# Performance work log

Hardware: AMD Instinct MI355X
Metric: run time of the kernel (lower is better)

The kernel has to match this reference:

```python
import jax, jax.numpy as jnp
import numpy as np

C_CT, C_MRI, C_OUT = 64, 64, 64
B, D, H, W = 1, 8, 32, 32


def setup_inputs() -> dict:
    key = jax.random.key(0)
    ks = jax.random.split(key, 18)
    s = 0.05
    inp = {
        "ct_features": jax.random.normal(ks[0], (B, C_CT, D, H, W), jnp.float32),
        "mri_features": jax.random.normal(ks[1], (B, C_MRI, D, H, W), jnp.float32),
        # 1x1x1 Conv3d == per-voxel linear: weight (out, in), bias (out,)
        "wq_ct": jax.random.normal(ks[2], (C_OUT, C_CT), jnp.float32) * s,
        "bq_ct": jax.random.normal(ks[3], (C_OUT,), jnp.float32) * s,
        "wk_mri": jax.random.normal(ks[4], (C_OUT, C_MRI), jnp.float32) * s,
        "bk_mri": jax.random.normal(ks[5], (C_OUT,), jnp.float32) * s,
        "wv_mri": jax.random.normal(ks[6], (C_OUT, C_MRI), jnp.float32) * s,
        "bv_mri": jax.random.normal(ks[7], (C_OUT,), jnp.float32) * s,
        "wq_mri": jax.random.normal(ks[8], (C_OUT, C_MRI), jnp.float32) * s,
        "bq_mri": jax.random.normal(ks[9], (C_OUT,), jnp.float32) * s,
        "wk_ct": jax.random.normal(ks[10], (C_OUT, C_CT), jnp.float32) * s,
        "bk_ct": jax.random.normal(ks[11], (C_OUT,), jnp.float32) * s,
        "wv_ct": jax.random.normal(ks[12], (C_OUT, C_CT), jnp.float32) * s,
        "bv_ct": jax.random.normal(ks[13], (C_OUT,), jnp.float32) * s,
        "wo": jax.random.normal(ks[14], (C_OUT, 2 * C_OUT), jnp.float32) * s,
        "bo": jax.random.normal(ks[15], (C_OUT,), jnp.float32) * s,
    }
    return inp


def _proj(x_flat, w, b):
    # x_flat: (B, Cin, N); 1x1x1 conv -> (B, Cout, N)
    return jnp.einsum("oc,bcn->bon", w, x_flat) + b[None, :, None]


def _forward(ct, mri, wq_ct, bq_ct, wk_mri, bk_mri, wv_mri, bv_mri,
             wq_mri, bq_mri, wk_ct, bk_ct, wv_ct, bv_ct, wo, bo):
    b, _, d, h, w = ct.shape
    n = d * h * w
    ct_f = ct.reshape(b, ct.shape[1], n)
    mri_f = mri.reshape(b, mri.shape[1], n)
    scale = 1.0 / np.sqrt(C_OUT).astype(np.float32)

    # CT queries attend over MRI keys/values
    ct_q = _proj(ct_f, wq_ct, bq_ct)      # (B, C, N)
    mri_k = _proj(mri_f, wk_mri, bk_mri)  # (B, C, N)
    mri_v = _proj(mri_f, wv_mri, bv_mri)  # (B, C, N)
    attn_ct = jax.nn.softmax(jnp.einsum("bci,bcj->bij", ct_q, mri_k) * scale, axis=-1)
    ct_att = jnp.einsum("bcj,bij->bci", mri_v, attn_ct)  # (B, C, N)

    # MRI queries attend over CT keys/values
    mri_q = _proj(mri_f, wq_mri, bq_mri)
    ct_k = _proj(ct_f, wk_ct, bk_ct)
    ct_v = _proj(ct_f, wv_ct, bv_ct)
    attn_mri = jax.nn.softmax(jnp.einsum("bci,bcj->bij", mri_q, ct_k) * scale, axis=-1)
    mri_att = jnp.einsum("bcj,bij->bci", ct_v, attn_mri)

    fused = jnp.concatenate([ct_att, mri_att], axis=1)  # (B, 2C, N)
    out = _proj(fused, wo, bo)  # (B, C, N)
    return out.reshape(b, C_OUT, d, h, w)


def reference(ct_features, mri_features, wq_ct, bq_ct, wk_mri, bk_mri,
              wv_mri, bv_mri, wq_mri, bq_mri, wk_ct, bk_ct, wv_ct, bv_ct,
              wo, bo):
    return _forward(ct_features, mri_features, wq_ct, bq_ct, wk_mri, bk_mri,
                    wv_mri, bv_mri, wq_mri, bq_mri, wk_ct, bk_ct,
                    wv_ct, bv_ct, wo, bo)
```

## Files before the change

### kernel.cpp

```cpp
#include <hip/hip_runtime.h>
#include <stdint.h>

constexpr int N = 8192;
constexpr float QSCALE = 0.18033688011112042f;
constexpr int SPLIT = 4;

typedef __attribute__((ext_vector_type(4))) float f32x4;
typedef __attribute__((ext_vector_type(4))) unsigned int u32x4;
typedef __attribute__((ext_vector_type(2))) unsigned int u32x2;
typedef __attribute__((ext_vector_type(4))) unsigned short u16x4;

__device__ inline unsigned short f2bf(float f) {
  unsigned u = __builtin_bit_cast(unsigned, f);
  u += 0x7FFFu + ((u >> 16) & 1u);
  return (unsigned short)(u >> 16);
}
__device__ inline float bf2f(unsigned short u) {
  return __builtin_bit_cast(float, (unsigned)u << 16);
}
__device__ inline unsigned cvtpk(float a, float b) {
  unsigned r;
  asm("v_cvt_pk_bf16_f32 %0, %1, %2" : "=v"(r) : "v"(a), "v"(b));
  return r;
}

__device__ inline void mfma16x16x32bf16(f32x4& d, u32x4 a, u32x4 b) {
  asm volatile("v_mfma_f32_16x16x32_bf16 %0, %1, %2, %0" : "+v"(d) : "v"(a), "v"(b));
}
__device__ inline void mfma_guard() {
  __builtin_amdgcn_sched_barrier(0);
  asm volatile("s_nop 7\n\ts_nop 7");
  __builtin_amdgcn_sched_barrier(0);
}
__device__ inline void gload16(const void* src, void* lds) {
  __builtin_amdgcn_global_load_lds(
      (const __attribute__((address_space(1))) unsigned int*)src,
      (__attribute__((address_space(3))) unsigned int*)lds, 16, 0, 0);
}

struct ProjArgs {
  const float* x[6];
  const float* w[6];
  const float* b[6];
  unsigned short* o[6];
  int mode[6];
  float scale[6];
};

__global__ __launch_bounds__(256) void proj_kernel(ProjArgs A) {
  const int p = blockIdx.y;
  const float* __restrict__ x = A.x[p];
  const float* __restrict__ w = A.w[p];
  const float* __restrict__ bias = A.b[p];
  unsigned short* __restrict__ out = A.o[p];
  const int n0 = blockIdx.x * 64;
  __shared__ float Xs[64][64];
  __shared__ float Ws[64][64];
  const int t = threadIdx.x;
#pragma unroll
  for (int i = 0; i < 4; i++) {
    int s = t + i * 256;
    ((u32x4*)Ws)[s] = ((const u32x4*)w)[s];
  }
#pragma unroll
  for (int i = 0; i < 4; i++) {
    int s = t + i * 256;
    int c = s >> 4, nc = s & 15;
    *(u32x4*)&Xs[c][nc * 4] = *(const u32x4*)&x[c * N + n0 + nc * 4];
  }
  __syncthreads();
  const int n = t & 63, h = t >> 6;
  float acc[16];
#pragma unroll
  for (int o = 0; o < 16; o++) acc[o] = bias[h * 16 + o];
  for (int c = 0; c < 64; c++) {
    float xv = Xs[c][n];
#pragma unroll
    for (int o = 0; o < 16; o++) acc[o] = fmaf(Ws[h * 16 + o][c], xv, acc[o]);
  }
  const float sc = A.scale[p];
  if (A.mode[p] == 0) {
    unsigned short* po = out + (size_t)(n0 + n) * 64 + h * 16;
#pragma unroll
    for (int o = 0; o < 16; o++) po[o] = f2bf(acc[o] * sc);
  } else {
#pragma unroll
    for (int o = 0; o < 16; o++) out[(size_t)(h * 16 + o) * N + n0 + n] = f2bf(acc[o] * sc);
  }
}

__global__ __launch_bounds__(256, 3) void attn_kernel(
    const unsigned short* __restrict__ Q0, const unsigned short* __restrict__ K0,
    const unsigned short* __restrict__ V0, const unsigned short* __restrict__ Q1,
    const unsigned short* __restrict__ K1, const unsigned short* __restrict__ V1,
    unsigned short* __restrict__ Opart, float* __restrict__ Lsum) {
  const int bid = blockIdx.x;
  const int slice = bid & 7;
  const int qb = bid >> 3;
  const int dir = slice >> 2;
  const int chunk = slice & 3;
  const unsigned short* __restrict__ Q = dir ? Q1 : Q0;
  const unsigned short* __restrict__ K = dir ? K1 : K0;
  const unsigned short* __restrict__ V = dir ? V1 : V0;

  __shared__ char smem[49152];

  const int t = threadIdx.x;
  const int lane = t & 63, w = t >> 6;
  const int g = lane >> 4, sl = lane & 15;
  char* const pw = smem + 32768 + w * 4096;
  const int kvbase = chunk * 2048;
  const int qswz = (sl & 7) << 4;

  const int srowoff = lane >> 3;
  const int swzb = ((lane & 7) ^ (lane >> 3)) * 16;
  const char* const Kc = (const char*)K;
  const char* const Vc = (const char*)V;

#define STAGE(jtile, slot)                                                     \
  do {                                                                         \
    const int j0s = kvbase + (jtile) * 64;                                     \
    _Pragma("unroll") for (int i = 0; i < 2; i++) {                            \
      const int row = (w * 2 + i) * 8 + srowoff;                               \
      gload16(Kc + (size_t)(j0s + row) * 128 + swzb,                           \
              smem + (slot) * 8192 + (w * 2 + i) * 1024);                      \
      gload16(Vc + (size_t)row * (N * 2) + (size_t)j0s * 2 + swzb,             \
              smem + 16384 + (slot) * 8192 + (w * 2 + i) * 1024);              \
    }                                                                          \
  } while (0)

  u32x4 qf[2][2];
#pragma unroll
  for (int rb = 0; rb < 2; rb++) {
    const int qrow = qb * 128 + w * 32 + rb * 16 + sl;
#pragma unroll
    for (int ks = 0; ks < 2; ks++)
      qf[rb][ks] = *(const u32x4*)(Q + (size_t)qrow * 64 + ks * 32 + 8 * g);
  }

  f32x4 acc[4][2];
#pragma unroll
  for (int mb = 0; mb < 4; mb++)
#pragma unroll
    for (int rb = 0; rb < 2; rb++)
#pragma unroll
      for (int r = 0; r < 4; r++) acc[mb][rb][r] = 0.f;
  float lpart[2] = {0.f, 0.f};

  STAGE(0, 0);
  for (int jt = 0; jt < 32; ++jt) {
    asm volatile("s_waitcnt vmcnt(0)" ::: "memory");
    __builtin_amdgcn_s_barrier();
    __builtin_amdgcn_sched_barrier(0);
    const int cur = jt & 1;
    if (jt + 1 < 32) STAGE(jt + 1, cur ^ 1);
    char* const Kl = smem + cur * 8192;
    char* const Vl = smem + 16384 + cur * 8192;

    u32x4 kf[4][2];
#pragma unroll
    for (int jb = 0; jb < 4; jb++) {
      const int row = jb * 16 + sl;
      const int rs = (row & 7) << 4;
#pragma unroll
      for (int ks = 0; ks < 2; ks++)
        kf[jb][ks] = *(const u32x4*)(Kl + row * 128 + ((ks * 64 + 16 * g) ^ rs));
    }

    f32x4 st[4][2];
    __builtin_amdgcn_s_setprio(1);
#pragma unroll
    for (int jb = 0; jb < 4; jb++)
#pragma unroll
      for (int rb = 0; rb < 2; rb++) {
#pragma unroll
        for (int r = 0; r < 4; r++) st[jb][rb][r] = 0.f;
        mfma16x16x32bf16(st[jb][rb], kf[jb][0], qf[rb][0]);
        mfma16x16x32bf16(st[jb][rb], kf[jb][1], qf[rb][1]);
      }
    __builtin_amdgcn_s_setprio(0);
    mfma_guard();

    u32x4 vf[4][2];
#pragma unroll
    for (int mb = 0; mb < 4; mb++) {
      const int row = mb * 16 + sl;
      const int rs = (row & 7) << 4;
#pragma unroll
      for (int ks = 0; ks < 2; ks++)
        vf[mb][ks] = *(const u32x4*)(Vl + row * 128 + ((ks * 64 + 16 * g) ^ rs));
    }

#pragma unroll
    for (int rb = 0; rb < 2; rb++) {
#pragma unroll
      for (int jb = 0; jb < 4; jb++) {
        float e0 = __builtin_amdgcn_exp2f(st[jb][rb][0]);
        float e1 = __builtin_amdgcn_exp2f(st[jb][rb][1]);
        float e2 = __builtin_amdgcn_exp2f(st[jb][rb][2]);
        float e3 = __builtin_amdgcn_exp2f(st[jb][rb][3]);
        lpart[rb] += (e0 + e1) + (e2 + e3);
        u32x2 pk;
        pk[0] = cvtpk(e0, e1);
        pk[1] = cvtpk(e2, e3);
        *(u32x2*)(pw + rb * 2048 + sl * 128 + ((jb * 32 + 8 * g) ^ qswz)) = pk;
      }
    }

#pragma unroll
    for (int rb = 0; rb < 2; rb++) {
      u32x4 pf0 = *(const u32x4*)(pw + rb * 2048 + sl * 128 + ((16 * g) ^ qswz));
      u32x4 pf1 = *(const u32x4*)(pw + rb * 2048 + sl * 128 + ((64 + 16 * g) ^ qswz));
      __builtin_amdgcn_s_setprio(1);
#pragma unroll
      for (int mb = 0; mb < 4; mb++) {
        mfma16x16x32bf16(acc[mb][rb], vf[mb][0], pf0);
        mfma16x16x32bf16(acc[mb][rb], vf[mb][1], pf1);
      }
      __builtin_amdgcn_s_setprio(0);
    }
  }
#undef STAGE
  mfma_guard();

#pragma unroll
  for (int rb = 0; rb < 2; rb++) {
    lpart[rb] += __shfl_xor(lpart[rb], 16);
    lpart[rb] += __shfl_xor(lpart[rb], 32);
  }

#pragma unroll
  for (int rb = 0; rb < 2; rb++) {
    const int q = rb * 16 + sl;
    const int qg = qb * 128 + w * 32 + q;
    const size_t pbase = ((size_t)slice * N + qg) * 64;
#pragma unroll
    for (int mb = 0; mb < 4; mb++) {
      u32x2 pk;
      pk[0] = cvtpk(acc[mb][rb][0], acc[mb][rb][1]);
      pk[1] = cvtpk(acc[mb][rb][2], acc[mb][rb][3]);
      *(u32x2*)(Opart + pbase + mb * 16 + 4 * g) = pk;
    }
    if (g == 0) Lsum[(size_t)slice * N + qg] = lpart[rb];
  }
}

__global__ __launch_bounds__(256) void oproj_kernel(
    const unsigned short* __restrict__ Opart, const float* __restrict__ Lsum,
    const float* __restrict__ wo, const float* __restrict__ bo,
    float* __restrict__ out) {
  __shared__ float Fs[128][32];
  __shared__ float Ws[64][128];
  const int t = threadIdx.x;
  const int n0 = blockIdx.x * 32;
#pragma unroll
  for (int i = 0; i < 8; i++) {
    int s = t + i * 256;
    ((u32x4*)Ws)[s] = ((const u32x4*)wo)[s];
  }
  const int q = t & 31;
  const int cg = t >> 5;
#pragma unroll
  for (int dir = 0; dir < 2; dir++) {
    float lt = 0.f;
#pragma unroll
    for (int c = 0; c < 4; c++) lt += Lsum[(size_t)(dir * SPLIT + c) * N + n0 + q];
    const float rD = 1.0f / lt;
#pragma unroll
    for (int i = 0; i < 2; i++) {
      const int ch4 = cg * 2 + i;
      float s0 = 0.f, s1 = 0.f, s2 = 0.f, s3 = 0.f;
#pragma unroll
      for (int c = 0; c < 4; c++) {
        u16x4 v = *(const u16x4*)(Opart +
            ((size_t)(dir * SPLIT + c) * N + n0 + q) * 64 + ch4 * 4);
        s0 += bf2f(v[0]); s1 += bf2f(v[1]); s2 += bf2f(v[2]); s3 += bf2f(v[3]);
      }
      Fs[dir * 64 + ch4 * 4 + 0][q] = s0 * rD;
      Fs[dir * 64 + ch4 * 4 + 1][q] = s1 * rD;
      Fs[dir * 64 + ch4 * 4 + 2][q] = s2 * rD;
      Fs[dir * 64 + ch4 * 4 + 3][q] = s3 * rD;
    }
  }
  __syncthreads();
  const int n = t & 31, h = t >> 5;
  float acc[8];
#pragma unroll
  for (int o = 0; o < 8; o++) acc[o] = bo[h * 8 + o];
  for (int ch = 0; ch < 128; ch++) {
    float fv = Fs[ch][n];
#pragma unroll
    for (int o = 0; o < 8; o++) acc[o] = fmaf(Ws[h * 8 + o][ch], fv, acc[o]);
  }
#pragma unroll
  for (int o = 0; o < 8; o++) out[(size_t)(h * 8 + o) * N + n0 + n] = acc[o];
}

extern "C" void kernel_launch(void* const* d_in, const int* in_sizes, int n_in,
                              void* d_out, int out_size, void* d_ws, size_t ws_size,
                              hipStream_t stream) {
  const float* ct     = (const float*)d_in[0];
  const float* mri    = (const float*)d_in[1];
  const float* wq_ct  = (const float*)d_in[2];
  const float* bq_ct  = (const float*)d_in[3];
  const float* wk_mri = (const float*)d_in[4];
  const float* bk_mri = (const float*)d_in[5];
  const float* wv_mri = (const float*)d_in[6];
  const float* bv_mri = (const float*)d_in[7];
  const float* wq_mri = (const float*)d_in[8];
  const float* bq_mri = (const float*)d_in[9];
  const float* wk_ct  = (const float*)d_in[10];
  const float* bk_ct  = (const float*)d_in[11];
  const float* wv_ct  = (const float*)d_in[12];
  const float* bv_ct  = (const float*)d_in[13];
  const float* wo     = (const float*)d_in[14];
  const float* bo     = (const float*)d_in[15];

  char* ws = (char*)d_ws;
  const size_t MB = (size_t)1 << 20;
  unsigned short* Qt_ct  = (unsigned short*)(ws + 0 * MB);
  unsigned short* Kt_mri = (unsigned short*)(ws + 1 * MB);
  unsigned short* V_mri  = (unsigned short*)(ws + 2 * MB);
  unsigned short* Qt_mri = (unsigned short*)(ws + 3 * MB);
  unsigned short* Kt_ct  = (unsigned short*)(ws + 4 * MB);
  unsigned short* V_ct   = (unsigned short*)(ws + 5 * MB);
  unsigned short* Opart  = (unsigned short*)(ws + 6 * MB);
  float* Lsum            = (float*)(ws + 14 * MB);

  ProjArgs A;
  A.x[0] = ct;  A.w[0] = wq_ct;  A.b[0] = bq_ct;  A.o[0] = Qt_ct;  A.mode[0] = 0; A.scale[0] = QSCALE;
  A.x[1] = mri; A.w[1] = wk_mri; A.b[1] = bk_mri; A.o[1] = Kt_mri; A.mode[1] = 0; A.scale[1] = 1.f;
  A.x[2] = mri; A.w[2] = wv_mri; A.b[2] = bv_mri; A.o[2] = V_mri;  A.mode[2] = 1; A.scale[2] = 1.f;
  A.x[3] = mri; A.w[3] = wq_mri; A.b[3] = bq_mri; A.o[3] = Qt_mri; A.mode[3] = 0; A.scale[3] = QSCALE;
  A.x[4] = ct;  A.w[4] = wk_ct;  A.b[4] = bk_ct;  A.o[4] = Kt_ct;  A.mode[4] = 0; A.scale[4] = 1.f;
  A.x[5] = ct;  A.w[5] = wv_ct;  A.b[5] = bv_ct;  A.o[5] = V_ct;   A.mode[5] = 1; A.scale[5] = 1.f;

  proj_kernel<<<dim3(128, 6), 256, 0, stream>>>(A);
  attn_kernel<<<dim3(512), 256, 0, stream>>>(Qt_ct, Kt_mri, V_mri,
                                             Qt_mri, Kt_ct, V_ct, Opart, Lsum);
  oproj_kernel<<<dim3(256), 256, 0, stream>>>(Opart, Lsum, wo, bo, (float*)d_out);
}
```

Measured before the change: 73.05 us.

## Switch attention kernel to 32x32x16 MFMA with register-resident P via permlane swap

Moves the attention kernel from 16x16x32 to 32x32x16 bf16 MFMA tiles and splits work so each wave owns a 64-query by 32-key sub-tile. Softmax probabilities are repacked in registers with v_permlane32_swap instead of a round trip through LDS, which drops the per-wave P buffer. Because the two key-half waves each hold partial outputs, a cross-wave reduction through LDS is added at the end. Launch bounds drop from 3 to 2 blocks per SIMD target to make room for the larger accumulators.

```diff
diff --git a/kernel.cpp b/kernel.cpp
--- a/kernel.cpp
+++ b/kernel.cpp
@@ -6,6 +6,7 @@
 constexpr int SPLIT = 4;
 
 typedef __attribute__((ext_vector_type(4))) float f32x4;
+typedef __attribute__((ext_vector_type(16))) float f32x16;
 typedef __attribute__((ext_vector_type(4))) unsigned int u32x4;
 typedef __attribute__((ext_vector_type(2))) unsigned int u32x2;
 typedef __attribute__((ext_vector_type(4))) unsigned short u16x4;
@@ -24,8 +25,8 @@
   return r;
 }
 
-__device__ inline void mfma16x16x32bf16(f32x4& d, u32x4 a, u32x4 b) {
-  asm volatile("v_mfma_f32_16x16x32_bf16 %0, %1, %2, %0" : "+v"(d) : "v"(a), "v"(b));
+__device__ inline void mfma32(f32x16& d, u32x4 a, u32x4 b) {
+  asm volatile("v_mfma_f32_32x32x16_bf16 %0, %1, %2, %0" : "+v"(d) : "v"(a), "v"(b));
 }
 __device__ inline void mfma_guard() {
   __builtin_amdgcn_sched_barrier(0);
@@ -89,7 +90,7 @@
   }
 }
 
-__global__ __launch_bounds__(256, 3) void attn_kernel(
+__global__ __launch_bounds__(256, 2) void attn_kernel(
     const unsigned short* __restrict__ Q0, const unsigned short* __restrict__ K0,
     const unsigned short* __restrict__ V0, const unsigned short* __restrict__ Q1,
     const unsigned short* __restrict__ K1, const unsigned short* __restrict__ V1,
@@ -103,14 +104,13 @@
   const unsigned short* __restrict__ K = dir ? K1 : K0;
   const unsigned short* __restrict__ V = dir ? V1 : V0;
 
-  __shared__ char smem[49152];
+  __shared__ char smem[33280];
 
   const int t = threadIdx.x;
   const int lane = t & 63, w = t >> 6;
-  const int g = lane >> 4, sl = lane & 15;
-  char* const pw = smem + 32768 + w * 4096;
+  const int qsub = w >> 1, jsub = w & 1;
+  const int hi = lane >> 5, l31 = lane & 31;
   const int kvbase = chunk * 2048;
-  const int qswz = (sl & 7) << 4;
 
   const int srowoff = lane >> 3;
   const int swzb = ((lane & 7) ^ (lane >> 3)) * 16;
@@ -129,22 +129,22 @@
     }                                                                          \
   } while (0)
 
-  u32x4 qf[2][2];
-#pragma unroll
-  for (int rb = 0; rb < 2; rb++) {
-    const int qrow = qb * 128 + w * 32 + rb * 16 + sl;
-#pragma unroll
-    for (int ks = 0; ks < 2; ks++)
-      qf[rb][ks] = *(const u32x4*)(Q + (size_t)qrow * 64 + ks * 32 + 8 * g);
-  }
-
-  f32x4 acc[4][2];
-#pragma unroll
-  for (int mb = 0; mb < 4; mb++)
-#pragma unroll
-    for (int rb = 0; rb < 2; rb++)
-#pragma unroll
-      for (int r = 0; r < 4; r++) acc[mb][rb][r] = 0.f;
+  u32x4 qf[2][4];
+#pragma unroll
+  for (int qs = 0; qs < 2; qs++) {
+    const int qrow = qb * 128 + qsub * 64 + qs * 32 + l31;
+#pragma unroll
+    for (int ks = 0; ks < 4; ks++)
+      qf[qs][ks] = *(const u32x4*)((const char*)Q + (size_t)qrow * 128 + (2 * ks + hi) * 16);
+  }
+
+  f32x16 acc[2][2];
+#pragma unroll
+  for (int cb = 0; cb < 2; cb++)
+#pragma unroll
+    for (int qs = 0; qs < 2; qs++)
+#pragma unroll
+      for (int r = 0; r < 16; r++) acc[cb][qs][r] = 0.f;
   float lpart[2] = {0.f, 0.f};
 
   STAGE(0, 0);
@@ -157,66 +157,63 @@
     char* const Kl = smem + cur * 8192;
     char* const Vl = smem + 16384 + cur * 8192;
 
-    u32x4 kf[4][2];
-#pragma unroll
-    for (int jb = 0; jb < 4; jb++) {
-      const int row = jb * 16 + sl;
+    u32x4 kf[4];
+    {
+      const int row = jsub * 32 + l31;
       const int rs = (row & 7) << 4;
 #pragma unroll
-      for (int ks = 0; ks < 2; ks++)
-        kf[jb][ks] = *(const u32x4*)(Kl + row * 128 + ((ks * 64 + 16 * g) ^ rs));
-    }
-
-    f32x4 st[4][2];
+      for (int ks = 0; ks < 4; ks++)
+        kf[ks] = *(const u32x4*)(Kl + row * 128 + (((2 * ks + hi) * 16) ^ rs));
+    }
+
+    f32x16 st[2];
+#pragma unroll
+    for (int qs = 0; qs < 2; qs++)
+#pragma unroll
+      for (int r = 0; r < 16; r++) st[qs][r] = 0.f;
     __builtin_amdgcn_s_setprio(1);
 #pragma unroll
-    for (int jb = 0; jb < 4; jb++)
-#pragma unroll
-      for (int rb = 0; rb < 2; rb++) {
-#pragma unroll
-        for (int r = 0; r < 4; r++) st[jb][rb][r] = 0.f;
-        mfma16x16x32bf16(st[jb][rb], kf[jb][0], qf[rb][0]);
-        mfma16x16x32bf16(st[jb][rb], kf[jb][1], qf[rb][1]);
-      }
+    for (int ks = 0; ks < 4; ks++) {
+      mfma32(st[0], kf[ks], qf[0][ks]);
+      mfma32(st[1], kf[ks], qf[1][ks]);
+    }
     __builtin_amdgcn_s_setprio(0);
     mfma_guard();
 
-    u32x4 vf[4][2];
-#pragma unroll
-    for (int mb = 0; mb < 4; mb++) {
-      const int row = mb * 16 + sl;
+    u32x4 vf[2][2];
+#pragma unroll
+    for (int cb = 0; cb < 2; cb++) {
+      const int row = cb * 32 + l31;
       const int rs = (row & 7) << 4;
 #pragma unroll
-      for (int ks = 0; ks < 2; ks++)
-        vf[mb][ks] = *(const u32x4*)(Vl + row * 128 + ((ks * 64 + 16 * g) ^ rs));
-    }
-
-#pragma unroll
-    for (int rb = 0; rb < 2; rb++) {
-#pragma unroll
-      for (int jb = 0; jb < 4; jb++) {
-        float e0 = __builtin_amdgcn_exp2f(st[jb][rb][0]);
-        float e1 = __builtin_amdgcn_exp2f(st[jb][rb][1]);
-        float e2 = __builtin_amdgcn_exp2f(st[jb][rb][2]);
-        float e3 = __builtin_amdgcn_exp2f(st[jb][rb][3]);
-        lpart[rb] += (e0 + e1) + (e2 + e3);
-        u32x2 pk;
-        pk[0] = cvtpk(e0, e1);
-        pk[1] = cvtpk(e2, e3);
-        *(u32x2*)(pw + rb * 2048 + sl * 128 + ((jb * 32 + 8 * g) ^ qswz)) = pk;
-      }
-    }
-
-#pragma unroll
-    for (int rb = 0; rb < 2; rb++) {
-      u32x4 pf0 = *(const u32x4*)(pw + rb * 2048 + sl * 128 + ((16 * g) ^ qswz));
-      u32x4 pf1 = *(const u32x4*)(pw + rb * 2048 + sl * 128 + ((64 + 16 * g) ^ qswz));
+      for (int js = 0; js < 2; js++)
+        vf[cb][js] = *(const u32x4*)(Vl + row * 128 + (((jsub * 4 + js * 2 + hi) * 16) ^ rs));
+    }
+
+#pragma unroll
+    for (int qs = 0; qs < 2; qs++) {
+      float p[16];
+#pragma unroll
+      for (int r = 0; r < 16; r++) p[r] = __builtin_amdgcn_exp2f(st[qs][r]);
+      lpart[qs] += (((p[0] + p[1]) + (p[2] + p[3])) + ((p[4] + p[5]) + (p[6] + p[7]))) +
+                   (((p[8] + p[9]) + (p[10] + p[11])) + ((p[12] + p[13]) + (p[14] + p[15])));
+      unsigned w00 = cvtpk(p[0], p[1]),   w01 = cvtpk(p[2], p[3]);
+      unsigned w10 = cvtpk(p[4], p[5]),   w11 = cvtpk(p[6], p[7]);
+      unsigned w20 = cvtpk(p[8], p[9]),   w21 = cvtpk(p[10], p[11]);
+      unsigned w30 = cvtpk(p[12], p[13]), w31 = cvtpk(p[14], p[15]);
+      asm volatile("v_permlane32_swap_b32 %0, %1" : "+v"(w00), "+v"(w10));
+      asm volatile("v_permlane32_swap_b32 %0, %1" : "+v"(w01), "+v"(w11));
+      asm volatile("v_permlane32_swap_b32 %0, %1" : "+v"(w20), "+v"(w30));
+      asm volatile("v_permlane32_swap_b32 %0, %1" : "+v"(w21), "+v"(w31));
+      u32x4 pf0, pf1;
+      pf0[0] = w00; pf0[1] = w01; pf0[2] = w10; pf0[3] = w11;
+      pf1[0] = w20; pf1[1] = w21; pf1[2] = w30; pf1[3] = w31;
+      mfma_guard();
       __builtin_amdgcn_s_setprio(1);
-#pragma unroll
-      for (int mb = 0; mb < 4; mb++) {
-        mfma16x16x32bf16(acc[mb][rb], vf[mb][0], pf0);
-        mfma16x16x32bf16(acc[mb][rb], vf[mb][1], pf1);
-      }
+      mfma32(acc[0][qs], vf[0][0], pf0);
+      mfma32(acc[1][qs], vf[1][0], pf0);
+      mfma32(acc[0][qs], vf[0][1], pf1);
+      mfma32(acc[1][qs], vf[1][1], pf1);
       __builtin_amdgcn_s_setprio(0);
     }
   }
@@ -224,24 +221,50 @@
   mfma_guard();
 
 #pragma unroll
-  for (int rb = 0; rb < 2; rb++) {
-    lpart[rb] += __shfl_xor(lpart[rb], 16);
-    lpart[rb] += __shfl_xor(lpart[rb], 32);
-  }
-
-#pragma unroll
-  for (int rb = 0; rb < 2; rb++) {
-    const int q = rb * 16 + sl;
-    const int qg = qb * 128 + w * 32 + q;
-    const size_t pbase = ((size_t)slice * N + qg) * 64;
-#pragma unroll
-    for (int mb = 0; mb < 4; mb++) {
-      u32x2 pk;
-      pk[0] = cvtpk(acc[mb][rb][0], acc[mb][rb][1]);
-      pk[1] = cvtpk(acc[mb][rb][2], acc[mb][rb][3]);
-      *(u32x2*)(Opart + pbase + mb * 16 + 4 * g) = pk;
-    }
-    if (g == 0) Lsum[(size_t)slice * N + qg] = lpart[rb];
+  for (int qs = 0; qs < 2; qs++) lpart[qs] += __shfl_xor(lpart[qs], 32);
+
+  __syncthreads();
+  char* const obuf = smem + qsub * 16384;
+  float* const mlb = (float*)(smem + 32768);
+  if (jsub == 1) {
+#pragma unroll
+    for (int qs = 0; qs < 2; qs++) {
+      const int qloc = qs * 32 + l31;
+      const int qsw = (qloc & 7) << 4;
+#pragma unroll
+      for (int cb = 0; cb < 2; cb++)
+#pragma unroll
+        for (int a = 0; a < 4; a++) {
+          const int ch0 = cb * 32 + 8 * a + 4 * hi;
+          f32x4 v;
+          v[0] = acc[cb][qs][4 * a];     v[1] = acc[cb][qs][4 * a + 1];
+          v[2] = acc[cb][qs][4 * a + 2]; v[3] = acc[cb][qs][4 * a + 3];
+          *(f32x4*)(obuf + qloc * 256 + ((ch0 * 4) ^ qsw)) = v;
+        }
+      if (hi == 0) mlb[qsub * 64 + qloc] = lpart[qs];
+    }
+  }
+  __syncthreads();
+  if (jsub == 0) {
+#pragma unroll
+    for (int qs = 0; qs < 2; qs++) {
+      const int qloc = qs * 32 + l31;
+      const int qsw = (qloc & 7) << 4;
+      const int qg = qb * 128 + qsub * 64 + qloc;
+      const size_t pbase = ((size_t)slice * N + qg) * 64;
+#pragma unroll
+      for (int cb = 0; cb < 2; cb++)
+#pragma unroll
+        for (int a = 0; a < 4; a++) {
+          const int ch0 = cb * 32 + 8 * a + 4 * hi;
+          f32x4 oo = *(const f32x4*)(obuf + qloc * 256 + ((ch0 * 4) ^ qsw));
+          u32x2 pk;
+          pk[0] = cvtpk(acc[cb][qs][4 * a] + oo[0], acc[cb][qs][4 * a + 1] + oo[1]);
+          pk[1] = cvtpk(acc[cb][qs][4 * a + 2] + oo[2], acc[cb][qs][4 * a + 3] + oo[3]);
+          *(u32x2*)(Opart + pbase + ch0) = pk;
+        }
+      if (hi == 0) Lsum[(size_t)slice * N + qg] = lpart[qs] + mlb[qsub * 64 + qloc];
+    }
   }
 }
 
```

After: 69.83 us. 4.4% less time.
